# Performance work log

Hardware: AMD Instinct MI355X
Metric: run time of the kernel (lower is better)

## Reference

```python
import jax, jax.numpy as jnp
import numpy as np

B, L, C, H, V = 64, 512, 256, 4, 32000
D = C // H
DIL = (1, 2, 4)
WIN = 3
NC = (50, 20)
NEG = -1e9


def setup_inputs() -> dict:
    key = jax.random.key(0)
    ks = jax.random.split(key, 20)
    g = lambda i, shape: jax.random.normal(ks[i], shape, jnp.float32) * 0.05
    Lay = len(DIL)
    x = jax.random.randint(ks[0], (B, L), 0, V)
    emb = g(1, (V, C)).at[0].set(0.0)  # padding_idx=0 row is zero
    return dict(
        x=x, emb=emb, pos=g(2, (L, C)),
        gp_W=g(3, (Lay, C, C)), gp_as=g(4, (Lay, H, D)), gp_ad=g(5, (Lay, H, D)),
        gf_W=g(6, (Lay, C, C)), gf_as=g(7, (Lay, H, D)), gf_ad=g(8, (Lay, H, D)),
        msg_W=g(9, (Lay, C, 2 * C)), msg_b=jnp.zeros((Lay, C), jnp.float32),
        gru_Wih=g(10, (Lay, 3 * C, C)), gru_bih=jnp.zeros((Lay, 3 * C), jnp.float32),
        gru_Whh=g(11, (Lay, 3 * C, C)), gru_bhh=jnp.zeros((Lay, 3 * C), jnp.float32),
        ln_g=jnp.ones((Lay, C), jnp.float32), ln_b=jnp.zeros((Lay, C), jnp.float32),
        pool_w=g(12, (C,)), pool_b=jnp.zeros((), jnp.float32),
        h0_W=g(13, (NC[0], C)), h0_b=jnp.zeros((NC[0],), jnp.float32),
        h1_W=g(14, (NC[1], C)), h1_b=jnp.zeros((NC[1],), jnp.float32),
    )


def _dense_gat(x, W, a_src, a_dst, adj):
    # x: [B,L,C], W: [C_out,C_in], a_*: [H,D], adj: [B,L,L] bool
    b, l, _ = x.shape
    h = jnp.einsum('blc,oc->blo', x, W).reshape(b, l, H, D).transpose(0, 2, 1, 3)  # [B,H,L,D]
    s = jnp.einsum('bhld,hd->bhl', h, a_src)
    d = jnp.einsum('bhld,hd->bhl', h, a_dst)
    e = s[:, :, :, None] + d[:, :, None, :]            # [B,H,L,L]
    e = jnp.where(e > 0, e, 0.2 * e)                   # LeakyReLU(0.2)
    e = jnp.where(adj[:, None, :, :], e, NEG)
    alpha = jax.nn.softmax(e, axis=-1)                 # dropout is identity in eval
    out = jnp.einsum('bhij,bhjd->bhid', alpha, h)
    return out.transpose(0, 2, 1, 3).reshape(b, l, C)


def _forward(x, emb, pos, gp_W, gp_as, gp_ad, gf_W, gf_as, gf_ad,
             msg_W, msg_b, gru_Wih, gru_bih, gru_Whh, gru_bhh,
             ln_g, ln_b, pool_w, pool_b, h0_W, h0_b, h1_W, h1_b):
    mask = x != 0                                      # [B,L]
    mf = mask.astype(jnp.float32)[..., None]           # [B,L,1]
    h = (emb[x] + pos[None, :, :] * mf) * mf
    logical = jnp.clip(jnp.cumsum(mask.astype(jnp.int32), axis=1) - 1, 0)
    valid = mask[:, None, :] & mask[:, :, None]        # [B,L,L]
    eye = jnp.eye(L, dtype=bool)[None]
    for l in range(len(DIL)):
        dil = DIL[l]
        diff = logical[:, :, None] - logical[:, None, :]
        ad = jnp.abs(diff)
        in_win = (ad <= WIN * dil) & (ad % dil == 0)
        adj_p = (valid & in_win & (diff < 0)) | eye
        adj_f = (valid & in_win & (diff > 0)) | eye
        m_p = _dense_gat(h, gp_W[l], gp_as[l], gp_ad[l], adj_p)
        m_f = _dense_gat(h, gf_W[l], gf_as[l], gf_ad[l], adj_f)
        m = jnp.concatenate([m_p, m_f], axis=-1)
        m = jax.nn.relu(jnp.einsum('blk,ck->blc', m, msg_W[l]) + msg_b[l])
        # GRUCell(input=m, hidden=h), PyTorch gate order: r,z,n
        gi = jnp.einsum('blc,gc->blg', m, gru_Wih[l]) + gru_bih[l]
        gh = jnp.einsum('blc,gc->blg', h, gru_Whh[l]) + gru_bhh[l]
        ir, iz, inn = jnp.split(gi, 3, axis=-1)
        hr, hz, hn = jnp.split(gh, 3, axis=-1)
        r = jax.nn.sigmoid(ir + hr)
        z = jax.nn.sigmoid(iz + hz)
        n = jnp.tanh(inn + r * hn)
        h_new = (1.0 - z) * n + z * h
        mu = jnp.mean(h_new, axis=-1, keepdims=True)
        var = jnp.mean(jnp.square(h_new - mu), axis=-1, keepdims=True)
        h_new = (h_new - mu) * jax.lax.rsqrt(var + 1e-5) * ln_g[l] + ln_b[l]
        h = h_new * mf
    # attention pooling over sequence (masked softmax on linear scores)
    sc = jnp.einsum('blc,c->bl', h, pool_w) + pool_b
    sc = jnp.where(mask, sc, NEG)
    a = jax.nn.softmax(sc, axis=-1)
    pooled = jnp.einsum('bl,blc->bc', a, h)            # dropout identity in eval
    o0 = pooled @ h0_W.T + h0_b
    o1 = pooled @ h1_W.T + h1_b
    return jnp.concatenate([o0, o1], axis=-1)          # [B, 50+20]


def reference(x, emb, pos, gp_W, gp_as, gp_ad, gf_W, gf_as, gf_ad,
              msg_W, msg_b, gru_Wih, gru_bih, gru_Whh, gru_bhh,
              ln_g, ln_b, pool_w, pool_b, h0_W, h0_b, h1_W, h1_b):
    return _forward(x, emb, pos, gp_W, gp_as, gp_ad, gf_W, gf_as, gf_ad,
                    msg_W, msg_b, gru_Wih, gru_bih, gru_Whh, gru_bhh,
                    ln_g, ln_b, pool_w, pool_b, h0_W, h0_b, h1_W, h1_b)
```

## Files before the change

kernel.cpp:

```cpp
#include <hip/hip_runtime.h>
#include <math.h>

#define B_ 64
#define L_ 512
#define C_ 256
#define H_ 4
#define LAY 3
#define NEGV -1e9f

typedef __attribute__((ext_vector_type(8))) short short8;
typedef __attribute__((ext_vector_type(4))) short short4v;
typedef __attribute__((ext_vector_type(4))) float floatx4;

static __device__ __forceinline__ float rcp_(float x) { return __builtin_amdgcn_rcpf(x); }
static __device__ __forceinline__ float sig_(float x) { return rcp_(1.f + __expf(-x)); }
static __device__ __forceinline__ float tanh_(float x) {
    float e = __expf(2.f * x);
    return 1.f - 2.f * rcp_(e + 1.f);
}

static __device__ __forceinline__ short f2bf(float f) {
    unsigned x = __float_as_uint(f);
    x += 0x7fffu + ((x >> 16) & 1u);
    return (short)(x >> 16);
}
static __device__ __forceinline__ float bf2f(short s) {
    return __uint_as_float(((unsigned)(unsigned short)s) << 16);
}

static __device__ __forceinline__ int tok_swizzle(int blk) {
    int c8 = blk & 7, i = blk >> 3;
    return (c8 + 8 * (i >> 5)) * 128 + (i & 31) * 4;
}

static __device__ __forceinline__ void gl_lds16(const short* g, short* l) {
    __builtin_amdgcn_global_load_lds(
        (const __attribute__((address_space(1))) unsigned int*)g,
        (__attribute__((address_space(3))) unsigned int*)l, 16, 0, 0);
}

#define CF() asm volatile("" ::: "memory")

#define PR_N0 (3 * 640 * 256)
#define PR_N1 (3 * 256 * 512)
#define PR_N2 (3 * 1024 * 512)
#define PR_N3 (3 * 1024)
#define PR_N4 (B_ * 70)
#define PR_TOT (PR_N0 + PR_N1 + PR_N2 + PR_N3 + PR_N4)

__global__ void prep_all(const float* __restrict__ gpW, const float* __restrict__ gfW,
                         const float* __restrict__ gpas, const float* __restrict__ gpad,
                         const float* __restrict__ gfas, const float* __restrict__ gfad,
                         const float* __restrict__ msgW,
                         const float* __restrict__ Wih, const float* __restrict__ Whh,
                         const float* __restrict__ bih, const float* __restrict__ bhh,
                         short* __restrict__ Wc, short* __restrict__ msgWb,
                         short* __restrict__ Bc, float* __restrict__ bias4,
                         float* __restrict__ outz) {
    int i = blockIdx.x * 256 + threadIdx.x;
    if (i < PR_N0) {
        int k = i & 255;
        int r = (i >> 8) % 640;
        int l = i / (640 * 256);
        float v = 0.f;
        if (r < 256) {
            v = gpW[((size_t)l * 256 + r) * 256 + k];
        } else if (r < 512) {
            v = gfW[((size_t)l * 256 + (r - 256)) * 256 + k];
        } else {
            int n = r - 512;
            if (n < 16) {
                int type = n >> 3, dir = (n >> 2) & 1, hh = n & 3;
                const float* a = type ? (dir ? gfad : gpad) : (dir ? gfas : gpas);
                const float* W = dir ? gfW : gpW;
                for (int j = 0; j < 64; j++) {
                    float av = a[l * 256 + hh * 64 + j];
                    float wv = W[((size_t)l * 256 + hh * 64 + j) * 256 + k];
                    v = fmaf(av, wv, v);
                }
            }
        }
        Wc[i] = f2bf(v);
        return;
    }
    i -= PR_N0;
    if (i < PR_N1) { msgWb[i] = f2bf(msgW[i]); return; }
    i -= PR_N1;
    if (i < PR_N2) {
        int k = i & 511, np = (i >> 9) & 1023, l = i >> 19;
        int ch = np >> 2, g = np & 3;
        float v = 0.f;
        if (g < 2) {
            v = (k < 256) ? Wih[((size_t)l * 768 + g * 256 + ch) * 256 + k]
                          : Whh[((size_t)l * 768 + g * 256 + ch) * 256 + (k - 256)];
        } else if (g == 2) {
            if (k < 256) v = Wih[((size_t)l * 768 + 512 + ch) * 256 + k];
        } else {
            if (k >= 256) v = Whh[((size_t)l * 768 + 512 + ch) * 256 + (k - 256)];
        }
        Bc[i] = f2bf(v);
        return;
    }
    i -= PR_N2;
    if (i < PR_N3) {
        int np = i & 1023, l = i >> 10;
        int ch = np >> 2, g = np & 3;
        float v;
        if (g < 2)       v = bih[l * 768 + g * 256 + ch] + bhh[l * 768 + g * 256 + ch];
        else if (g == 2) v = bih[l * 768 + 512 + ch];
        else             v = bhh[l * 768 + 512 + ch];
        bias4[i] = v;
        return;
    }
    i -= PR_N3;
    if (i < PR_N4) outz[i] = 0.f;
}

__global__ __launch_bounds__(512) void scan_embed(
    const int* __restrict__ x, const float* __restrict__ emb,
    const float* __restrict__ pos, short* __restrict__ hb,
    int* __restrict__ mask, int* __restrict__ logical,
    int* __restrict__ pol, int* __restrict__ nvalid) {
    if (blockIdx.x < 64) {
        int b = blockIdx.x, t = threadIdx.x;
        __shared__ int s[L_];
        int m = (x[b * L_ + t] != 0) ? 1 : 0;
        s[t] = m;
        __syncthreads();
        for (int off = 1; off < L_; off <<= 1) {
            int v = (t >= off) ? s[t - off] : 0;
            __syncthreads();
            s[t] += v;
            __syncthreads();
        }
        int cum = s[t];
        int lg = cum - 1; if (lg < 0) lg = 0;
        mask[b * L_ + t] = m;
        logical[b * L_ + t] = lg;
        if (m) pol[b * L_ + lg] = t;
        if (t == L_ - 1) nvalid[b] = cum;
    } else {
        int t = threadIdx.x & 255, sub = threadIdx.x >> 8;
        int blk2 = (blockIdx.x - 64) * 2 + sub;
        int bl = tok_swizzle(blk2) + (t >> 6);
        int lane = t & 63;
        int xv = x[bl];
        float mf = (xv != 0) ? 1.f : 0.f;
        int l = bl & (L_ - 1);
        float4 e = *(const float4*)&emb[(size_t)xv * C_ + lane * 4];
        float4 p = *(const float4*)&pos[(size_t)l * C_ + lane * 4];
        short4v hv4;
        hv4.x = f2bf((e.x + p.x * mf) * mf);
        hv4.y = f2bf((e.y + p.y * mf) * mf);
        hv4.z = f2bf((e.z + p.z * mf) * mf);
        hv4.w = f2bf((e.w + p.w * mf) * mf);
        *(short4v*)&hb[(size_t)bl * C_ + lane * 4] = hv4;
    }
}

static __device__ __forceinline__ short8 lds_rd8(const short* p) {
    return *(const short8*)p;
}

template <int MH>
static __device__ __forceinline__ void ld_af(const short* bufA, int wm, int q, int t16,
                                             short8 af[4][2]) {
#pragma unroll
    for (int mfl = 0; mfl < 4; ++mfl) {
        int row = wm * 128 + (MH * 4 + mfl) * 16 + t16;
#pragma unroll
        for (int ks = 0; ks < 2; ++ks) {
            int cg = (ks * 4 + q) ^ (row & 7);
            af[mfl][ks] = lds_rd8(&bufA[row * 64 + cg * 8]);
        }
    }
}

template <int NH>
static __device__ __forceinline__ void ld_bf(const short* bufB, int wn, int q, int t16,
                                             short8 bf[2][2]) {
#pragma unroll
    for (int nfl = 0; nfl < 2; ++nfl) {
        int row = wn * 64 + (NH * 2 + nfl) * 16 + t16;
#pragma unroll
        for (int ks = 0; ks < 2; ++ks) {
            int cg = (ks * 4 + q) ^ (row & 7);
            bf[nfl][ks] = lds_rd8(&bufB[row * 64 + cg * 8]);
        }
    }
}

static __device__ __forceinline__ void ld_bf32(const short* bufB, int wn, int q, int t16,
                                               short8 bf[2][2]) {
#pragma unroll
    for (int nfl = 0; nfl < 2; ++nfl) {
        int row = wn * 32 + nfl * 16 + t16;
#pragma unroll
        for (int ks = 0; ks < 2; ++ks) {
            int cg = (ks * 4 + q) ^ (row & 7);
            bf[nfl][ks] = lds_rd8(&bufB[row * 64 + cg * 8]);
        }
    }
}

template <int MH, int NH>
static __device__ __forceinline__ void mfma_q(const short8 af[4][2], const short8 bf[2][2],
                                              floatx4 acc[4][8]) {
    __builtin_amdgcn_s_setprio(1);
#pragma unroll
    for (int ks = 0; ks < 2; ++ks)
#pragma unroll
        for (int mfl = 0; mfl < 4; ++mfl)
#pragma unroll
            for (int nfl = 0; nfl < 2; ++nfl)
                acc[NH * 2 + nfl][MH * 4 + mfl] = __builtin_amdgcn_mfma_f32_16x16x32_bf16(
                    bf[nfl][ks], af[mfl][ks], acc[NH * 2 + nfl][MH * 4 + mfl], 0, 0, 0);
    __builtin_amdgcn_s_setprio(0);
}

template <int MH>
static __device__ __forceinline__ void mfma_m(const short8 af[4][2], const short8 bf[2][2],
                                              floatx4 acc[2][8]) {
    __builtin_amdgcn_s_setprio(1);
#pragma unroll
    for (int ks = 0; ks < 2; ++ks)
#pragma unroll
        for (int mfl = 0; mfl < 4; ++mfl)
#pragma unroll
            for (int nfl = 0; nfl < 2; ++nfl)
                acc[nfl][MH * 4 + mfl] = __builtin_amdgcn_mfma_f32_16x16x32_bf16(
                    bf[nfl][ks], af[mfl][ks], acc[nfl][MH * 4 + mfl], 0, 0, 0);
    __builtin_amdgcn_s_setprio(0);
}

__global__ __launch_bounds__(512, 2) void projssd_deep(const short* __restrict__ A0,
                                                       const short* __restrict__ Bw,
                                                       short* __restrict__ hpb2,
                                                       float* __restrict__ Ssd) {
    __shared__ short lds[2][24576];
    const int id = blockIdx.x;
    const int j = id >> 3;
    const int cb = j >> 4;
    const int rb = (id & 7) * 16 + (j & 15);
    const int tid = threadIdx.x;
    const int wave = tid >> 6, lane = tid & 63;
    const int wm = wave >> 2, wn = wave & 3;
    const int q = lane >> 4, t16 = lane & 15;
    const size_t arow0 = (size_t)rb * 256;
    const short* Bb = Bw + (size_t)cb * 128 * 256;

    floatx4 acc[2][8];
#pragma unroll
    for (int i = 0; i < 2; i++)
#pragma unroll
        for (int jj = 0; jj < 8; jj++) acc[i][jj] = (floatx4)0.f;

    auto stageA = [&](int t, int Hh) {
        short* bufA = lds[t & 1];
#pragma unroll
        for (int u = 0; u < 2; ++u) {
            int unit = u * 512 + tid;
            int row = Hh * 128 + (unit >> 3);
            int cs = (unit & 7) ^ (row & 7);
            gl_lds16(A0 + (arow0 + (size_t)row) * 256 + t * 64 + cs * 8,
                     bufA + Hh * 8192 + unit * 8);
        }
    };
    auto stageB = [&](int t) {
        short* bufB = lds[t & 1] + 16384;
#pragma unroll
        for (int u = 0; u < 2; ++u) {
            int unit = u * 512 + tid;
            int row = unit >> 3;
            int cs = (unit & 7) ^ (row & 7);
            gl_lds16(Bb + (size_t)row * 256 + t * 64 + cs * 8, bufB + unit * 8);
        }
    };

    stageA(0, 0); stageA(0, 1); stageB(0); stageB(1);
    asm volatile("s_waitcnt vmcnt(2)" ::: "memory");
    CF(); __builtin_amdgcn_s_barrier(); CF();

    short8 af[4][2], bfr[2][2];

#pragma unroll
    for (int t = 0; t < 4; ++t) {
        const short* bufA = lds[t & 1];
        const short* bufB = lds[t & 1] + 16384;

        ld_af<0>(bufA, wm, q, t16, af);
        ld_bf32(bufB, wn, q, t16, bfr);
        if (t < 3) { stageA(t + 1, 0); stageA(t + 1, 1); }
        CF(); __builtin_amdgcn_s_barrier();
        asm volatile("s_waitcnt lgkmcnt(0)" ::: "memory");
        __builtin_amdgcn_sched_barrier(0);
        mfma_m<0>(af, bfr, acc);
        CF(); __builtin_amdgcn_s_barrier(); CF();

        ld_af<1>(bufA, wm, q, t16, af);
        if (t < 2) stageB(t + 2);
        CF(); __builtin_amdgcn_s_barrier();
        asm volatile("s_waitcnt lgkmcnt(0)" ::: "memory");
        __builtin_amdgcn_sched_barrier(0);
        mfma_m<1>(af, bfr, acc);
        if (t < 2)       asm volatile("s_waitcnt vmcnt(2)" ::: "memory");
        else if (t == 2) asm volatile("s_waitcnt vmcnt(0)" ::: "memory");
        CF(); __builtin_amdgcn_s_barrier(); CF();
    }

    if (cb < 4) {
        short* sO = (short*)lds;
#pragma unroll
        for (int nf = 0; nf < 2; nf++) {
            int chl = wn * 32 + nf * 16 + q * 4;
#pragma unroll
            for (int mf = 0; mf < 8; mf++) {
                int rowl = wm * 128 + mf * 16 + t16;
                short4v pk;
                pk.x = f2bf(acc[nf][mf][0]);
                pk.y = f2bf(acc[nf][mf][1]);
                pk.z = f2bf(acc[nf][mf][2]);
                pk.w = f2bf(acc[nf][mf][3]);
                *(short4v*)&sO[rowl * 132 + chl] = pk;
            }
        }
        __syncthreads();
#pragma unroll
        for (int it = 0; it < 8; ++it) {
            int unit = it * 512 + tid;
            int rowl = unit >> 4, ck = unit & 15;
            *(short8*)&hpb2[(arow0 + rowl) * 512 + cb * 128 + ck * 8] =
                *(const short8*)&sO[rowl * 132 + ck * 8];
        }
    } else {
        if (wn == 0) {
            int chl = q * 4;
            if (chl < 16) {
#pragma unroll
                for (int mf = 0; mf < 8; mf++) {
                    int rowl = wm * 128 + mf * 16 + t16;
                    float4 pk = make_float4(acc[0][mf][0], acc[0][mf][1],
                                            acc[0][mf][2], acc[0][mf][3]);
                    *(float4*)&Ssd[(arow0 + rowl) * 16 + chl] = pk;
                }
            }
        }
    }
}

__global__ __launch_bounds__(512, 2) void gru_bgemm(const short* __restrict__ mmb,
                                                    const short* __restrict__ hb_in,
                                                    const short* __restrict__ Bw,
                                                    short* __restrict__ hn2b,
                                                    const float* __restrict__ bias4) {
    __shared__ short lds[2][32768];
    const int id = blockIdx.x;
    const int rb = 16 * (id & 7) + (id >> 5);
    const int cb = (id >> 3) & 3;
    const int tid = threadIdx.x;
    const int wave = tid >> 6, lane = tid & 63;
    const int wm = wave >> 2, wn = wave & 3;
    const int q = lane >> 4, t16 = lane & 15;
    const size_t arow0 = (size_t)rb * 256;
    const short* Bb = Bw + (size_t)cb * 256 * 512;
    const int ord0 = (5 + cb) & 7;

    floatx4 acc[4][8];
#pragma unroll
    for (int i = 0; i < 4; i++)
#pragma unroll
        for (int jj = 0; jj < 8; jj++) acc[i][jj] = (floatx4)0.f;

    auto stageA = [&](int i, int Hh) {
        int tt = (ord0 + i) & 7;
        const short* Asrc = (tt < 4) ? (mmb + tt * 64) : (hb_in + (tt - 4) * 64);
        short* bufA = lds[i & 1];
#pragma unroll
        for (int u = 0; u < 2; ++u) {
            int unit = u * 512 + tid;
            int row = Hh * 128 + (unit >> 3);
            int cs = (unit & 7) ^ (row & 7);
            gl_lds16(Asrc + (arow0 + (size_t)row) * 256 + cs * 8,
                     bufA + Hh * 8192 + unit * 8);
        }
    };
    auto stageB = [&](int i, int Hh) {
        int tt = (ord0 + i) & 7;
        short* bufB = lds[i & 1] + 16384;
#pragma unroll
        for (int u = 0; u < 2; ++u) {
            int unit = u * 512 + tid;
            int row = Hh * 128 + (unit >> 3);
            int cs = (unit & 7) ^ (row & 7);
            gl_lds16(Bb + (size_t)row * 512 + tt * 64 + cs * 8,
                     bufB + Hh * 8192 + unit * 8);
        }
    };

    stageA(0, 0); stageA(0, 1); stageB(0, 0); stageB(0, 1);
    stageA(1, 0); stageA(1, 1); stageB(1, 0); stageB(1, 1);
    asm volatile("s_waitcnt vmcnt(8)" ::: "memory");
    CF(); __builtin_amdgcn_s_barrier(); CF();

    short8 af[4][2], b0[2][2], b1[2][2];

#pragma unroll
    for (int t = 0; t < 8; ++t) {
        const short* bufA = lds[t & 1];
        const short* bufB = lds[t & 1] + 16384;

        ld_af<0>(bufA, wm, q, t16, af);
        ld_bf<0>(bufB, wn, q, t16, b0);
        CF(); __builtin_amdgcn_s_barrier();
        asm volatile("s_waitcnt lgkmcnt(0)" ::: "memory");
        __builtin_amdgcn_sched_barrier(0);
        mfma_q<0, 0>(af, b0, acc);
        CF(); __builtin_amdgcn_s_barrier(); CF();

        ld_bf<1>(bufB, wn, q, t16, b1);
        CF(); __builtin_amdgcn_s_barrier();
        asm volatile("s_waitcnt lgkmcnt(0)" ::: "memory");
        __builtin_amdgcn_sched_barrier(0);
        mfma_q<0, 1>(af, b1, acc);
        CF(); __builtin_amdgcn_s_barrier(); CF();

        ld_af<1>(bufA, wm, q, t16, af);
        if (t < 6) { stageB(t + 2, 0); stageB(t + 2, 1); }
        CF(); __builtin_amdgcn_s_barrier();
        asm volatile("s_waitcnt lgkmcnt(0)" ::: "memory");
        __builtin_amdgcn_sched_barrier(0);
        mfma_q<1, 1>(af, b1, acc);
        CF(); __builtin_amdgcn_s_barrier(); CF();

        if (t < 6) { stageA(t + 2, 0); stageA(t + 2, 1); }
        CF(); __builtin_amdgcn_s_barrier();
        mfma_q<1, 0>(af, b0, acc);
        if (t < 6)       asm volatile("s_waitcnt vmcnt(8)" ::: "memory");
        else if (t == 6) asm volatile("s_waitcnt vmcnt(0)" ::: "memory");
        CF(); __builtin_amdgcn_s_barrier(); CF();
    }

    const short* hpt = lds[1];
    short* sO = (short*)lds;
#pragma unroll
    for (int nf = 0; nf < 4; nf++) {
        int chl = wn * 16 + nf * 4 + q;
        int col0 = cb * 256 + wn * 64 + nf * 16 + q * 4;
        float4 bv4 = *(const float4*)&bias4[col0];
#pragma unroll
        for (int mf = 0; mf < 8; mf++) {
            int rowl = wm * 128 + mf * 16 + t16;
            float hp = bf2f(hpt[rowl * 64 + (((chl >> 3) ^ (rowl & 7)) << 3) + (chl & 7)]);
            float r = sig_(acc[nf][mf][0] + bv4.x);
            float z = sig_(acc[nf][mf][1] + bv4.y);
            float nv = tanh_((acc[nf][mf][2] + bv4.z) + r * (acc[nf][mf][3] + bv4.w));
            sO[rowl * 72 + chl] = f2bf((1.f - z) * nv + z * hp);
        }
    }
    __syncthreads();
#pragma unroll
    for (int it = 0; it < 4; ++it) {
        int unit = it * 512 + tid;
        int rowl = unit >> 3, ck = unit & 7;
        *(short8*)&hn2b[(arow0 + rowl) * 256 + cb * 64 + ck * 8] =
            *(const short8*)&sO[rowl * 72 + ck * 8];
    }
}

__global__ __launch_bounds__(512, 2) void msg_bgemm(const short* __restrict__ A0,
                                                    const short* __restrict__ Bw,
                                                    short* __restrict__ Cout,
                                                    const float* __restrict__ bias) {
    __shared__ short lds[2][24576];
    const int id = blockIdx.x;
    const int j = id >> 3;
    const int rb = (id & 7) * 16 + (j & 15);
    const int cb = j >> 4;
    const int tid = threadIdx.x;
    const int wave = tid >> 6, lane = tid & 63;
    const int wm = wave >> 2, wn = wave & 3;
    const int q = lane >> 4, t16 = lane & 15;
    const size_t arow0 = (size_t)rb * 256;
    const short* Bb = Bw + (size_t)cb * 128 * 512;

    floatx4 acc[2][8];
#pragma unroll
    for (int i = 0; i < 2; i++)
#pragma unroll
        for (int jj = 0; jj < 8; jj++) acc[i][jj] = (floatx4)0.f;

    auto stageA = [&](int t, int Hh) {
        short* bufA = lds[t & 1];
#pragma unroll
        for (int u = 0; u < 2; ++u) {
            int unit = u * 512 + tid;
            int row = Hh * 128 + (unit >> 3);
            int cs = (unit & 7) ^ (row & 7);
            gl_lds16(A0 + (arow0 + (size_t)row) * 512 + t * 64 + cs * 8,
                     bufA + Hh * 8192 + unit * 8);
        }
    };
    auto stageB = [&](int t) {
        short* bufB = lds[t & 1] + 16384;
#pragma unroll
        for (int u = 0; u < 2; ++u) {
            int unit = u * 512 + tid;
            int row = unit >> 3;
            int cs = (unit & 7) ^ (row & 7);
            gl_lds16(Bb + (size_t)row * 512 + t * 64 + cs * 8, bufB + unit * 8);
        }
    };

    stageA(0, 0); stageA(0, 1); stageB(0); stageB(1);
    asm volatile("s_waitcnt vmcnt(2)" ::: "memory");
    CF(); __builtin_amdgcn_s_barrier(); CF();

    short8 af[4][2], bfr[2][2];

#pragma unroll 2
    for (int t = 0; t < 8; ++t) {
        const short* bufA = lds[t & 1];
        const short* bufB = lds[t & 1] + 16384;

        ld_af<0>(bufA, wm, q, t16, af);
        ld_bf32(bufB, wn, q, t16, bfr);
        if (t < 7) { stageA(t + 1, 0); stageA(t + 1, 1); }
        CF(); __builtin_amdgcn_s_barrier();
        asm volatile("s_waitcnt lgkmcnt(0)" ::: "memory");
        mfma_m<0>(af, bfr, acc);
        CF(); __builtin_amdgcn_s_barrier(); CF();

        ld_af<1>(bufA, wm, q, t16, af);
        if (t < 6) stageB(t + 2);
        CF(); __builtin_amdgcn_s_barrier();
        asm volatile("s_waitcnt lgkmcnt(0)" ::: "memory");
        mfma_m<1>(af, bfr, acc);
        if (t < 6)       asm volatile("s_waitcnt vmcnt(2)" ::: "memory");
        else if (t == 6) asm volatile("s_waitcnt vmcnt(0)" ::: "memory");
        CF(); __builtin_amdgcn_s_barrier(); CF();
    }

    short* sO = (short*)lds;
#pragma unroll
    for (int nf = 0; nf < 2; nf++) {
        int chl = wn * 32 + nf * 16 + q * 4;
        int col0 = cb * 128 + chl;
        float4 bv4 = *(const float4*)&bias[col0];
#pragma unroll
        for (int mf = 0; mf < 8; mf++) {
            int rowl = wm * 128 + mf * 16 + t16;
            short4v pk;
            pk.x = f2bf(fmaxf(acc[nf][mf][0] + bv4.x, 0.f));
            pk.y = f2bf(fmaxf(acc[nf][mf][1] + bv4.y, 0.f));
            pk.z = f2bf(fmaxf(acc[nf][mf][2] + bv4.z, 0.f));
            pk.w = f2bf(fmaxf(acc[nf][mf][3] + bv4.w, 0.f));
            *(short4v*)&sO[rowl * 132 + chl] = pk;
        }
    }
    __syncthreads();
#pragma unroll
    for (int it = 0; it < 8; ++it) {
        int unit = it * 512 + tid;
        int rowl = unit >> 4, ck = unit & 15;
        *(short8*)&Cout[(arow0 + rowl) * 256 + cb * 128 + ck * 8] =
            *(const short8*)&sO[rowl * 132 + ck * 8];
    }
}

__global__ __launch_bounds__(256) void ln_kernel(
    const short* __restrict__ hn2b, short* __restrict__ hb,
    const int* __restrict__ mask,
    const float* __restrict__ lng, const float* __restrict__ lnb) {
    int t = threadIdx.x;
    int bl = tok_swizzle(blockIdx.x) + (t >> 6);
    int lane = t & 63;
    short4v v4 = *(const short4v*)&hn2b[(size_t)bl * C_ + lane * 4];
    float v[4] = {bf2f(v4.x), bf2f(v4.y), bf2f(v4.z), bf2f(v4.w)};
    float s = (v[0] + v[1]) + (v[2] + v[3]);
    float ss = (v[0] * v[0] + v[1] * v[1]) + (v[2] * v[2] + v[3] * v[3]);
#pragma unroll
    for (int off = 32; off; off >>= 1) {
        s += __shfl_xor(s, off);
        ss += __shfl_xor(ss, off);
    }
    float mu = s * (1.f / 256.f);
    float var = ss * (1.f / 256.f) - mu * mu;
    float rstd = rsqrtf(fmaxf(var, 0.f) + 1e-5f);
    float4 lg = *(const float4*)&lng[lane * 4];
    float4 lb = *(const float4*)&lnb[lane * 4];
    float mfv = mask[bl] ? 1.f : 0.f;
    short4v yb;
    yb.x = f2bf(((v[0] - mu) * rstd * lg.x + lb.x) * mfv);
    yb.y = f2bf(((v[1] - mu) * rstd * lg.y + lb.y) * mfv);
    yb.z = f2bf(((v[2] - mu) * rstd * lg.z + lb.z) * mfv);
    yb.w = f2bf(((v[3] - mu) * rstd * lg.w + lb.w) * mfv);
    *(short4v*)&hb[(size_t)bl * C_ + lane * 4] = yb;
}

__global__ __launch_bounds__(256) void agg_fused(
    const short* __restrict__ hpb2, const float* __restrict__ S,
    const int* __restrict__ mask, const int* __restrict__ logical,
    const int* __restrict__ pol, const int* __restrict__ nvalid,
    short* __restrict__ m, int dil) {
    int t = threadIdx.x;
    int bl = tok_swizzle(blockIdx.x) + (t >> 6);
    int sub = t & 63;
    int dir = sub >> 5;
    int slot = sub & 31;
    int cb = slot * 8;
    int head = slot >> 3;
    int b = bl >> 9;

    int mi = mask[bl];
    int li = logical[bl];
    int nv = nvalid[b];
    int js[3]; int nn = 0;
    if (mi) {
#pragma unroll
        for (int k = 1; k <= 3; k++) {
            int lj = dir ? (li - k * dil) : (li + k * dil);
            if (lj >= 0 && lj < nv) js[nn++] = pol[b * L_ + lj];
        }
    }
    int sn = dir * 4 + head, dn = 8 + sn;
    float si = S[(size_t)bl * 16 + sn];
    float di = S[(size_t)bl * 16 + dn];
    float e0 = si + di; e0 = e0 > 0.f ? e0 : 0.2f * e0;
    float emax = e0, ev[3];
    for (int k = 0; k < nn; k++) {
        float djv = S[((size_t)(b * L_ + js[k])) * 16 + dn];
        float e = si + djv; e = e > 0.f ? e : 0.2f * e;
        ev[k] = e; emax = fmaxf(emax, e);
    }
    float w0 = __expf(e0 - emax), den = w0;
    float wv[3];
    for (int k = 0; k < nn; k++) { wv[k] = __expf(ev[k] - emax); den += wv[k]; }
    float rden = rcp_(den);

    size_t base = (size_t)bl * 512 + dir * 256 + cb;
    short8 vself = *(const short8*)&hpb2[base];
    float o[8];
#pragma unroll
    for (int j = 0; j < 8; j++) o[j] = w0 * bf2f(vself[j]);
    for (int k = 0; k < nn; k++) {
        short8 vn = *(const short8*)&hpb2[((size_t)(b * L_ + js[k])) * 512 + dir * 256 + cb];
#pragma unroll
        for (int j = 0; j < 8; j++) o[j] = fmaf(wv[k], bf2f(vn[j]), o[j]);
    }
    short8 ov;
#pragma unroll
    for (int j = 0; j < 8; j++) ov[j] = f2bf(o[j] * rden);
    *(short8*)&m[base] = ov;
}

__global__ __launch_bounds__(1024) void pool_head_ln(
    const short* __restrict__ hn2b, const int* __restrict__ mask,
    const float* __restrict__ pw, const float* __restrict__ pb,
    const float* __restrict__ lng2, const float* __restrict__ lnb2,
    const float* __restrict__ h0W, const float* __restrict__ h0b,
    const float* __restrict__ h1W, const float* __restrict__ h1b,
    float* __restrict__ out) {
    int b = blockIdx.x >> 2, s = blockIdx.x & 3;
    int t = threadIdx.x;
    int lane = t & 63, wave = t >> 6;
    __shared__ float sc[L_];
    __shared__ float muA[L_];
    __shared__ float rsA[L_];
    __shared__ float red[24];
    __shared__ float part[16][64];
    __shared__ float pooled[64];

    float4 wv = *(const float4*)&pw[lane * 4];
    float4 gv = *(const float4*)&lng2[lane * 4];
    float4 bv = *(const float4*)&lnb2[lane * 4];
    float pg0 = wv.x * gv.x, pg1 = wv.y * gv.y, pg2 = wv.z * gv.z, pg3 = wv.w * gv.w;
    float cG = (pg0 + pg1) + (pg2 + pg3);
    float cB = (wv.x * bv.x + wv.y * bv.y) + (wv.z * bv.z + wv.w * bv.w);
#pragma unroll
    for (int off = 32; off; off >>= 1) {
        cG += __shfl_xor(cG, off);
        cB += __shfl_xor(cB, off);
    }
    float pb0 = pb[0];

    for (int l = wave; l < L_; l += 16) {
        short4v hv = *(const short4v*)&hn2b[((size_t)b * L_ + l) * C_ + lane * 4];
        float h0 = bf2f(hv.x), h1 = bf2f(hv.y), h2 = bf2f(hv.z), h3 = bf2f(hv.w);
        float s1 = pg0 * h0 + pg1 * h1 + pg2 * h2 + pg3 * h3;
        float s2 = (h0 + h1) + (h2 + h3);
        float s3 = (h0 * h0 + h1 * h1) + (h2 * h2 + h3 * h3);
#pragma unroll
        for (int off = 32; off; off >>= 1) {
            s1 += __shfl_down(s1, off);
            s2 += __shfl_down(s2, off);
            s3 += __shfl_down(s3, off);
        }
        if (lane == 0) {
            float mu = s2 * (1.f / 256.f);
            float var = s3 * (1.f / 256.f) - mu * mu;
            float rstd = rsqrtf(fmaxf(var, 0.f) + 1e-5f);
            int mk = mask[b * L_ + l];
            sc[l] = mk ? (rstd * (s1 - mu * cG) + cB + pb0) : NEGV;
            muA[l] = mu;
            rsA[l] = mk ? rstd : 0.f;
        }
    }
    __syncthreads();

    float v = (t < L_) ? sc[t] : NEGV;
    float mx = v;
#pragma unroll
    for (int off = 32; off; off >>= 1) mx = fmaxf(mx, __shfl_down(mx, off));
    if (lane == 0) red[wave] = mx;
    __syncthreads();
    if (t == 0) {
        float g = red[0];
        for (int i = 1; i < 16; i++) g = fmaxf(g, red[i]);
        red[16] = g;
    }
    __syncthreads();
    float gmax = red[16];
    float e = (t < L_) ? __expf(v - gmax) : 0.f;
    float ssum = e;
#pragma unroll
    for (int off = 32; off; off >>= 1) ssum += __shfl_down(ssum, off);
    if (lane == 0) red[wave] = ssum;
    __syncthreads();
    if (t == 0) {
        float g = 0.f;
        for (int i = 0; i < 16; i++) g += red[i];
        red[17] = 1.f / g;
    }
    __syncthreads();
    float a = e * red[17];
    float arv = (t < L_) ? a * rsA[t] : 0.f;
    float amu = (t < L_) ? arv * muA[t] : 0.f;
    if (t < L_) sc[t] = arv;
#pragma unroll
    for (int off = 32; off; off >>= 1) amu += __shfl_down(amu, off);
    if (lane == 0) red[wave] = amu;
    __syncthreads();
    if (t == 0) {
        float g = 0.f;
        for (int i = 0; i < 16; i++) g += red[i];
        red[18] = g;
    }
    __syncthreads();

    {
        int c0 = t & 63, lw = t >> 6;
        const short* hcol = &hn2b[((size_t)b * L_ + lw * 32) * C_ + s * 64 + c0];
        const float* scg = &sc[lw * 32];
        float a0 = 0.f, a1 = 0.f;
        for (int l = 0; l < 32; l += 2) {
            a0 = fmaf(scg[l + 0], bf2f(hcol[(size_t)(l + 0) * C_]), a0);
            a1 = fmaf(scg[l + 1], bf2f(hcol[(size_t)(l + 1) * C_]), a1);
        }
        part[lw][c0] = a0 + a1;
    }
    __syncthreads();
    if (t < 64) {
        float p = 0.f;
        for (int i = 0; i < 16; i++) p += part[i][t];
        int c = s * 64 + t;
        pooled[t] = lng2[c] * (p - red[18]) + lnb2[c];
    }
    __syncthreads();

    for (int o = wave; o < 70; o += 16) {
        const float* W = (o < 50) ? (h0W + (size_t)o * C_) : (h1W + (size_t)(o - 50) * C_);
        float sv = pooled[lane] * W[s * 64 + lane];
#pragma unroll
        for (int off = 32; off; off >>= 1) sv += __shfl_down(sv, off);
        if (lane == 0) {
            float add = sv + ((s == 0) ? ((o < 50) ? h0b[o] : h1b[o - 50]) : 0.f);
            atomicAdd(&out[b * 70 + o], add);
        }
    }
}

extern "C" void kernel_launch(void* const* d_in, const int* in_sizes, int n_in,
                              void* d_out, int out_size, void* d_ws, size_t ws_size,
                              hipStream_t stream) {
    const int*   x    = (const int*)d_in[0];
    const float* emb  = (const float*)d_in[1];
    const float* pos  = (const float*)d_in[2];
    const float* gpW  = (const float*)d_in[3];
    const float* gpas = (const float*)d_in[4];
    const float* gpad = (const float*)d_in[5];
    const float* gfW  = (const float*)d_in[6];
    const float* gfas = (const float*)d_in[7];
    const float* gfad = (const float*)d_in[8];
    const float* msgW = (const float*)d_in[9];
    const float* msgb = (const float*)d_in[10];
    const float* Wih  = (const float*)d_in[11];
    const float* bih  = (const float*)d_in[12];
    const float* Whh  = (const float*)d_in[13];
    const float* bhh  = (const float*)d_in[14];
    const float* lng  = (const float*)d_in[15];
    const float* lnb  = (const float*)d_in[16];
    const float* pw   = (const float*)d_in[17];
    const float* pb   = (const float*)d_in[18];
    const float* h0W  = (const float*)d_in[19];
    const float* h0b  = (const float*)d_in[20];
    const float* h1W  = (const float*)d_in[21];
    const float* h1b  = (const float*)d_in[22];
    float* out = (float*)d_out;

    const size_t MW = 1024 * 1024;
    float* ws = (float*)d_ws;
    short* hn2b = (short*)ws;
    short* hb   = (short*)(ws + 8 * MW);
    short* mmb  = (short*)(ws + 12 * MW);
    float* Ssd  = ws + 12 * MW;
    short* hpb2 = (short*)(ws + 16 * MW);
    short* mb   = (short*)(ws + 24 * MW);
    short* Wcomb = (short*)(ws + 32 * MW);
    short* msgWb = Wcomb + 3 * 640 * 256;
    short* Bcat  = msgWb + 3 * 256 * 512;
    float* bias4 = (float*)(Bcat + 3 * 1024 * 512);
    int* mask    = (int*)(bias4 + 3 * 1024);
    int* logical = mask + B_ * L_;
    int* pol     = logical + B_ * L_;
    int* nvalid  = pol + B_ * L_;

    prep_all<<<(PR_TOT + 255) / 256, 256, 0, stream>>>(
        gpW, gfW, gpas, gpad, gfas, gfad, msgW, Wih, Whh, bih, bhh,
        Wcomb, msgWb, Bcat, bias4, out);

    scan_embed<<<64 + 4096, 512, 0, stream>>>(x, emb, pos, hb, mask, logical, pol, nvalid);

    const int DILS[LAY] = {1, 2, 4};

    for (int l = 0; l < LAY; l++) {
        int dil = DILS[l];
        projssd_deep<<<640, 512, 0, stream>>>(hb, Wcomb + (size_t)l * 640 * 256,
                                              hpb2, Ssd);
        agg_fused<<<8192, 256, 0, stream>>>(hpb2, Ssd, mask, logical, pol, nvalid, mb, dil);
        msg_bgemm<<<256, 512, 0, stream>>>(mb, msgWb + (size_t)l * 256 * 512,
                                           mmb, msgb + l * C_);
        gru_bgemm<<<512, 512, 0, stream>>>(mmb, hb, Bcat + (size_t)l * 1024 * 512,
                                           hn2b, bias4 + l * 1024);
        if (l < 2)
            ln_kernel<<<8192, 256, 0, stream>>>(hn2b, hb, mask, lng + l * C_, lnb + l * C_);
    }

    pool_head_ln<<<B_ * 4, 1024, 0, stream>>>(hn2b, mask, pw, pb,
                                              lng + 2 * C_, lnb + 2 * C_,
                                              h0W, h0b, h1W, h1b, out);
}
```

Measured before the change: 480.7 us.

## Fuse GAT neighbor aggregation into message GEMM A-operand staging

Removes the separate agg_fused kernel and computes the attention-weighted neighbor aggregation directly into the LDS A tile of the message GEMM, so the intermediate buffer is never written to or read back from global memory. The GEMM is retiled so each block covers 128 rows by all 256 output columns instead of 256 rows by 128, which means aggregation is not duplicated across column blocks. The cost is heavier per-block staging work (gathers and exps) inside the pipelined loop, which can stall the MFMA pipeline, plus a larger B tile in LDS.

```diff
diff --git a/kernel.cpp b/kernel.cpp
--- a/kernel.cpp
+++ b/kernel.cpp
@@ -233,6 +233,48 @@
     __builtin_amdgcn_s_setprio(0);
 }
 
+template <int MH>
+static __device__ __forceinline__ void ld_afm(const short* bufA, int wm, int q, int t16,
+                                              short8 af[2][2]) {
+#pragma unroll
+    for (int mfl = 0; mfl < 2; ++mfl) {
+        int row = wm * 64 + (MH * 2 + mfl) * 16 + t16;
+#pragma unroll
+        for (int ks = 0; ks < 2; ++ks) {
+            int cg = (ks * 4 + q) ^ (row & 7);
+            af[mfl][ks] = lds_rd8(&bufA[row * 64 + cg * 8]);
+        }
+    }
+}
+
+static __device__ __forceinline__ void ld_bfq4(const short* bufB, int wn, int q, int t16,
+                                               short8 bf[4][2]) {
+#pragma unroll
+    for (int nf = 0; nf < 4; ++nf) {
+        int row = wn * 64 + nf * 16 + t16;
+#pragma unroll
+        for (int ks = 0; ks < 2; ++ks) {
+            int cg = (ks * 4 + q) ^ (row & 7);
+            bf[nf][ks] = lds_rd8(&bufB[row * 64 + cg * 8]);
+        }
+    }
+}
+
+template <int MH>
+static __device__ __forceinline__ void mfma_am(const short8 af[2][2], const short8 bf[4][2],
+                                               floatx4 acc[4][4]) {
+    __builtin_amdgcn_s_setprio(1);
+#pragma unroll
+    for (int ks = 0; ks < 2; ++ks)
+#pragma unroll
+        for (int mfl = 0; mfl < 2; ++mfl)
+#pragma unroll
+            for (int nf = 0; nf < 4; ++nf)
+                acc[nf][MH * 2 + mfl] = __builtin_amdgcn_mfma_f32_16x16x32_bf16(
+                    bf[nf][ks], af[mfl][ks], acc[nf][MH * 2 + mfl], 0, 0, 0);
+    __builtin_amdgcn_s_setprio(0);
+}
+
 __global__ __launch_bounds__(512, 2) void projssd_deep(const short* __restrict__ A0,
                                                        const short* __restrict__ Bw,
                                                        short* __restrict__ hpb2,
@@ -467,103 +509,164 @@
     }
 }
 
-__global__ __launch_bounds__(512, 2) void msg_bgemm(const short* __restrict__ A0,
-                                                    const short* __restrict__ Bw,
-                                                    short* __restrict__ Cout,
-                                                    const float* __restrict__ bias) {
-    __shared__ short lds[2][24576];
+__global__ __launch_bounds__(512, 2) void aggmsg_bgemm(
+    const short* __restrict__ hpb2, const float* __restrict__ S,
+    const int* __restrict__ mask, const int* __restrict__ logical,
+    const int* __restrict__ pol, const int* __restrict__ nvalid,
+    const short* __restrict__ Bw, short* __restrict__ Cout,
+    const float* __restrict__ bias, int dil) {
+    __shared__ short lds[49152];
+    __shared__ int jsm[128][8];
     const int id = blockIdx.x;
-    const int j = id >> 3;
-    const int rb = (id & 7) * 16 + (j & 15);
-    const int cb = j >> 4;
+    const int rb = (id & 7) * 32 + (id >> 3);
     const int tid = threadIdx.x;
     const int wave = tid >> 6, lane = tid & 63;
     const int wm = wave >> 2, wn = wave & 3;
     const int q = lane >> 4, t16 = lane & 15;
-    const size_t arow0 = (size_t)rb * 256;
-    const short* Bb = Bw + (size_t)cb * 128 * 512;
-
-    floatx4 acc[2][8];
-#pragma unroll
-    for (int i = 0; i < 2; i++)
-#pragma unroll
-        for (int jj = 0; jj < 8; jj++) acc[i][jj] = (floatx4)0.f;
-
-    auto stageA = [&](int t, int Hh) {
-        short* bufA = lds[t & 1];
-#pragma unroll
-        for (int u = 0; u < 2; ++u) {
-            int unit = u * 512 + tid;
-            int row = Hh * 128 + (unit >> 3);
-            int cs = (unit & 7) ^ (row & 7);
-            gl_lds16(A0 + (arow0 + (size_t)row) * 512 + t * 64 + cs * 8,
-                     bufA + Hh * 8192 + unit * 8);
-        }
-    };
+    const int arow0 = rb * 128;
+    const int b = arow0 >> 9;
+
+    floatx4 acc[4][4];
+#pragma unroll
+    for (int i = 0; i < 4; i++)
+#pragma unroll
+        for (int jj = 0; jj < 4; jj++) acc[i][jj] = (floatx4)0.f;
+
     auto stageB = [&](int t) {
-        short* bufB = lds[t & 1] + 16384;
-#pragma unroll
-        for (int u = 0; u < 2; ++u) {
+        short* bufB = lds + 16384 + (t & 1) * 16384;
+#pragma unroll
+        for (int u = 0; u < 4; ++u) {
             int unit = u * 512 + tid;
             int row = unit >> 3;
             int cs = (unit & 7) ^ (row & 7);
-            gl_lds16(Bb + (size_t)row * 512 + t * 64 + cs * 8, bufB + unit * 8);
+            gl_lds16(Bw + (size_t)row * 512 + t * 64 + cs * 8, bufB + unit * 8);
         }
     };
 
-    stageA(0, 0); stageA(0, 1); stageB(0); stageB(1);
-    asm volatile("s_waitcnt vmcnt(2)" ::: "memory");
+    auto computeA = [&](int tt) {
+        short* bufA = lds + (tt & 1) * 8192;
+        int dir = tt >> 2, head = tt & 3;
+        int sn = dir * 4 + head, dn = 8 + sn;
+        int doff = dir * 256 + head * 64;
+#pragma unroll
+        for (int i = 0; i < 2; ++i) {
+            int unit = i * 512 + tid;
+            int row = unit >> 3, cb8 = unit & 7;
+            int j0 = jsm[row][dir * 3 + 0];
+            int j1 = jsm[row][dir * 3 + 1];
+            int j2 = jsm[row][dir * 3 + 2];
+            int tok = arow0 + row;
+            float si = S[(size_t)tok * 16 + sn];
+            float di = S[(size_t)tok * 16 + dn];
+            float e0 = si + di; e0 = e0 > 0.f ? e0 : 0.2f * e0;
+            float e1 = -1e30f, e2 = -1e30f, e3 = -1e30f;
+            if (j0 >= 0) { float e = si + S[(size_t)j0 * 16 + dn]; e1 = e > 0.f ? e : 0.2f * e; }
+            if (j1 >= 0) { float e = si + S[(size_t)j1 * 16 + dn]; e2 = e > 0.f ? e : 0.2f * e; }
+            if (j2 >= 0) { float e = si + S[(size_t)j2 * 16 + dn]; e3 = e > 0.f ? e : 0.2f * e; }
+            float emax = fmaxf(fmaxf(e0, e1), fmaxf(e2, e3));
+            float w0 = __expf(e0 - emax);
+            float w1 = (j0 >= 0) ? __expf(e1 - emax) : 0.f;
+            float w2 = (j1 >= 0) ? __expf(e2 - emax) : 0.f;
+            float w3 = (j2 >= 0) ? __expf(e3 - emax) : 0.f;
+            float rden = rcp_(((w0 + w1) + (w2 + w3)));
+            size_t cboff = (size_t)doff + cb8 * 8;
+            short8 v0 = *(const short8*)&hpb2[(size_t)tok * 512 + cboff];
+            float o[8];
+#pragma unroll
+            for (int jj = 0; jj < 8; jj++) o[jj] = w0 * bf2f(v0[jj]);
+            if (j0 >= 0) {
+                short8 vn = *(const short8*)&hpb2[(size_t)j0 * 512 + cboff];
+#pragma unroll
+                for (int jj = 0; jj < 8; jj++) o[jj] = fmaf(w1, bf2f(vn[jj]), o[jj]);
+            }
+            if (j1 >= 0) {
+                short8 vn = *(const short8*)&hpb2[(size_t)j1 * 512 + cboff];
+#pragma unroll
+                for (int jj = 0; jj < 8; jj++) o[jj] = fmaf(w2, bf2f(vn[jj]), o[jj]);
+            }
+            if (j2 >= 0) {
+                short8 vn = *(const short8*)&hpb2[(size_t)j2 * 512 + cboff];
+#pragma unroll
+                for (int jj = 0; jj < 8; jj++) o[jj] = fmaf(w3, bf2f(vn[jj]), o[jj]);
+            }
+            short8 ov;
+#pragma unroll
+            for (int jj = 0; jj < 8; jj++) ov[jj] = f2bf(o[jj] * rden);
+            *(short8*)&bufA[row * 64 + ((cb8 ^ (row & 7)) * 8)] = ov;
+        }
+    };
+
+    if (tid < 128) {
+        int tok = arow0 + tid;
+        int mi = mask[tok];
+        int li = logical[tok];
+        int nv = nvalid[b];
+#pragma unroll
+        for (int dir = 0; dir < 2; ++dir)
+#pragma unroll
+            for (int k = 1; k <= 3; ++k) {
+                int lj = dir ? (li - k * dil) : (li + k * dil);
+                int jg = (mi && lj >= 0 && lj < nv) ? (b * L_ + pol[b * L_ + lj]) : -1;
+                jsm[tid][dir * 3 + (k - 1)] = jg;
+            }
+        jsm[tid][6] = mi;
+    }
+    stageB(0); stageB(1);
+    __syncthreads();
+    computeA(0);
+    asm volatile("s_waitcnt vmcnt(4) lgkmcnt(0)" ::: "memory");
     CF(); __builtin_amdgcn_s_barrier(); CF();
 
-    short8 af[4][2], bfr[2][2];
-
-#pragma unroll 2
+    short8 af[2][2], bfq[4][2];
+
+#pragma unroll
     for (int t = 0; t < 8; ++t) {
-        const short* bufA = lds[t & 1];
-        const short* bufB = lds[t & 1] + 16384;
-
-        ld_af<0>(bufA, wm, q, t16, af);
-        ld_bf32(bufB, wn, q, t16, bfr);
-        if (t < 7) { stageA(t + 1, 0); stageA(t + 1, 1); }
+        const short* bufA = lds + (t & 1) * 8192;
+        const short* bufB = lds + 16384 + (t & 1) * 16384;
+
+        ld_afm<0>(bufA, wm, q, t16, af);
+        ld_bfq4(bufB, wn, q, t16, bfq);
+        if (t < 7) computeA(t + 1);
         CF(); __builtin_amdgcn_s_barrier();
         asm volatile("s_waitcnt lgkmcnt(0)" ::: "memory");
-        mfma_m<0>(af, bfr, acc);
+        __builtin_amdgcn_sched_barrier(0);
+        mfma_am<0>(af, bfq, acc);
         CF(); __builtin_amdgcn_s_barrier(); CF();
 
-        ld_af<1>(bufA, wm, q, t16, af);
+        ld_afm<1>(bufA, wm, q, t16, af);
         if (t < 6) stageB(t + 2);
         CF(); __builtin_amdgcn_s_barrier();
         asm volatile("s_waitcnt lgkmcnt(0)" ::: "memory");
-        mfma_m<1>(af, bfr, acc);
-        if (t < 6)       asm volatile("s_waitcnt vmcnt(2)" ::: "memory");
+        __builtin_amdgcn_sched_barrier(0);
+        mfma_am<1>(af, bfq, acc);
+        if (t < 6)       asm volatile("s_waitcnt vmcnt(4)" ::: "memory");
         else if (t == 6) asm volatile("s_waitcnt vmcnt(0)" ::: "memory");
         CF(); __builtin_amdgcn_s_barrier(); CF();
     }
 
-    short* sO = (short*)lds;
-#pragma unroll
-    for (int nf = 0; nf < 2; nf++) {
-        int chl = wn * 32 + nf * 16 + q * 4;
-        int col0 = cb * 128 + chl;
+    short* sO = lds;
+#pragma unroll
+    for (int nf = 0; nf < 4; nf++) {
+        int col0 = wn * 64 + nf * 16 + q * 4;
         float4 bv4 = *(const float4*)&bias[col0];
 #pragma unroll
-        for (int mf = 0; mf < 8; mf++) {
-            int rowl = wm * 128 + mf * 16 + t16;
+        for (int mf = 0; mf < 4; mf++) {
+            int rowl = wm * 64 + mf * 16 + t16;
             short4v pk;
             pk.x = f2bf(fmaxf(acc[nf][mf][0] + bv4.x, 0.f));
             pk.y = f2bf(fmaxf(acc[nf][mf][1] + bv4.y, 0.f));
             pk.z = f2bf(fmaxf(acc[nf][mf][2] + bv4.z, 0.f));
             pk.w = f2bf(fmaxf(acc[nf][mf][3] + bv4.w, 0.f));
-            *(short4v*)&sO[rowl * 132 + chl] = pk;
+            *(short4v*)&sO[rowl * 264 + col0] = pk;
         }
     }
     __syncthreads();
 #pragma unroll
     for (int it = 0; it < 8; ++it) {
         int unit = it * 512 + tid;
-        int rowl = unit >> 4, ck = unit & 15;
-        *(short8*)&Cout[(arow0 + rowl) * 256 + cb * 128 + ck * 8] =
-            *(const short8*)&sO[rowl * 132 + ck * 8];
+        int rowl = unit >> 5, ck = unit & 31;
+        *(short8*)&Cout[((size_t)arow0 + rowl) * 256 + ck * 8] =
+            *(const short8*)&sO[rowl * 264 + ck * 8];
     }
 }
 
@@ -595,62 +698,6 @@
     yb.z = f2bf(((v[2] - mu) * rstd * lg.z + lb.z) * mfv);
     yb.w = f2bf(((v[3] - mu) * rstd * lg.w + lb.w) * mfv);
     *(short4v*)&hb[(size_t)bl * C_ + lane * 4] = yb;
-}
-
-__global__ __launch_bounds__(256) void agg_fused(
-    const short* __restrict__ hpb2, const float* __restrict__ S,
-    const int* __restrict__ mask, const int* __restrict__ logical,
-    const int* __restrict__ pol, const int* __restrict__ nvalid,
-    short* __restrict__ m, int dil) {
-    int t = threadIdx.x;
-    int bl = tok_swizzle(blockIdx.x) + (t >> 6);
-    int sub = t & 63;
-    int dir = sub >> 5;
-    int slot = sub & 31;
-    int cb = slot * 8;
-    int head = slot >> 3;
-    int b = bl >> 9;
-
-    int mi = mask[bl];
-    int li = logical[bl];
-    int nv = nvalid[b];
-    int js[3]; int nn = 0;
-    if (mi) {
-#pragma unroll
-        for (int k = 1; k <= 3; k++) {
-            int lj = dir ? (li - k * dil) : (li + k * dil);
-            if (lj >= 0 && lj < nv) js[nn++] = pol[b * L_ + lj];
-        }
-    }
-    int sn = dir * 4 + head, dn = 8 + sn;
-    float si = S[(size_t)bl * 16 + sn];
-    float di = S[(size_t)bl * 16 + dn];
-    float e0 = si + di; e0 = e0 > 0.f ? e0 : 0.2f * e0;
-    float emax = e0, ev[3];
-    for (int k = 0; k < nn; k++) {
-        float djv = S[((size_t)(b * L_ + js[k])) * 16 + dn];
-        float e = si + djv; e = e > 0.f ? e : 0.2f * e;
-        ev[k] = e; emax = fmaxf(emax, e);
-    }
-    float w0 = __expf(e0 - emax), den = w0;
-    float wv[3];
-    for (int k = 0; k < nn; k++) { wv[k] = __expf(ev[k] - emax); den += wv[k]; }
-    float rden = rcp_(den);
-
-    size_t base = (size_t)bl * 512 + dir * 256 + cb;
-    short8 vself = *(const short8*)&hpb2[base];
-    float o[8];
-#pragma unroll
-    for (int j = 0; j < 8; j++) o[j] = w0 * bf2f(vself[j]);
-    for (int k = 0; k < nn; k++) {
-        short8 vn = *(const short8*)&hpb2[((size_t)(b * L_ + js[k])) * 512 + dir * 256 + cb];
-#pragma unroll
-        for (int j = 0; j < 8; j++) o[j] = fmaf(wv[k], bf2f(vn[j]), o[j]);
-    }
-    short8 ov;
-#pragma unroll
-    for (int j = 0; j < 8; j++) ov[j] = f2bf(o[j] * rden);
-    *(short8*)&m[base] = ov;
 }
 
 __global__ __launch_bounds__(1024) void pool_head_ln(
@@ -814,7 +861,6 @@
     short* mmb  = (short*)(ws + 12 * MW);
     float* Ssd  = ws + 12 * MW;
     short* hpb2 = (short*)(ws + 16 * MW);
-    short* mb   = (short*)(ws + 24 * MW);
     short* Wcomb = (short*)(ws + 32 * MW);
     short* msgWb = Wcomb + 3 * 640 * 256;
     short* Bcat  = msgWb + 3 * 256 * 512;
@@ -836,9 +882,9 @@
         int dil = DILS[l];
         projssd_deep<<<640, 512, 0, stream>>>(hb, Wcomb + (size_t)l * 640 * 256,
                                               hpb2, Ssd);
-        agg_fused<<<8192, 256, 0, stream>>>(hpb2, Ssd, mask, logical, pol, nvalid, mb, dil);
-        msg_bgemm<<<256, 512, 0, stream>>>(mb, msgWb + (size_t)l * 256 * 512,
-                                           mmb, msgb + l * C_);
+        aggmsg_bgemm<<<256, 512, 0, stream>>>(hpb2, Ssd, mask, logical, pol, nvalid,
+                                              msgWb + (size_t)l * 256 * 512,
+                                              mmb, msgb + l * C_, dil);
         gru_bgemm<<<512, 512, 0, stream>>>(mmb, hb, Bcat + (size_t)l * 1024 * 512,
                                            hn2b, bias4 + l * 1024);
         if (l < 2)
```

Result: slower. 512.3 us (+6.6%).
